# Optimization experiments

Measured on AMD Instinct MI355X. Metric: run time of the kernel, lower is better.

## Reference

```python
import jax, jax.numpy as jnp
import numpy as np
import math

VOCAB = 50257
DIM = 2048
R = 64
SCALING = 128.0 / math.sqrt(R)  # use_rslora=True -> alpha/sqrt(r) = 16.0


def setup_inputs() -> dict:
    key = jax.random.key(0)
    k1, k2, k3 = jax.random.split(key, 3)
    x = jax.random.randint(k1, (4, 4096), 0, VOCAB)
    weight = jax.random.normal(k2, (VOCAB, DIM), dtype=jnp.float32)
    # lora_A init: normal(0, 1/sqrt(r)); lora_B init: zeros (use randn here so
    # the LoRA path is numerically exercised)
    lora_A = jax.random.normal(k3, (R, VOCAB), dtype=jnp.float32) / math.sqrt(R)
    lora_B = jax.random.normal(jax.random.fold_in(key, 7), (DIM, R), dtype=jnp.float32) * 0.02
    return {"x": x, "weight": weight, "lora_A": lora_A, "lora_B": lora_B}


def reference(x, weight, lora_A, lora_B):
    # base embedding gather: [B, S, D]
    base_embed = weight[x]
    # Mathematically identical to F.embedding(x, (lora_B @ lora_A).T):
    # gather columns of lora_A by token id, then project with lora_B.
    a_rows = lora_A.T[x]                       # [B, S, r]
    lora_embed = jnp.einsum('bsr,dr->bsd', a_rows, lora_B)  # [B, S, D]
    return base_embed + lora_embed * SCALING
```

## Files before the change

kernel.cpp:

```cpp
#include <hip/hip_runtime.h>


constexpr int VOCAB = 50257;
constexpr int DIM = 2048;
constexpr int R = 64;
constexpr float SCALING = 16.0f;
constexpr int T_TILE = 64;
constexpr int BLOCK = 256;

__global__ void gather_a_kernel(const int* __restrict__ x,
                                const float* __restrict__ lora_A,
                                float* __restrict__ a_rows,
                                int n_tokens) {
  int gid = blockIdx.x * blockDim.x + threadIdx.x;
  if (gid >= n_tokens * R) return;
  int t = gid >> 6;
  int r = gid & (R - 1);
  int tok = x[t];
  a_rows[gid] = lora_A[(size_t)r * VOCAB + (size_t)tok];
}

template <bool USE_WS>
__global__ void fused_kernel(const int* __restrict__ x,
                             const float* __restrict__ weight,
                             const float* __restrict__ lora_A,
                             const float* __restrict__ a_rows,
                             const float* __restrict__ lora_B,
                             float* __restrict__ out) {
  const int d = blockIdx.y * BLOCK + threadIdx.x;
  const int t0 = blockIdx.x * T_TILE;

  float b[R];
  const float* bp = lora_B + (size_t)d * R;
#pragma unroll
  for (int i = 0; i < R; i += 4) {
    float4 v = *reinterpret_cast<const float4*>(bp + i);
    b[i] = v.x; b[i + 1] = v.y; b[i + 2] = v.z; b[i + 3] = v.w;
  }

#pragma unroll 1
  for (int tt = 0; tt < T_TILE; ++tt) {
    const int t = t0 + tt;
    const int tok = x[t];

    float a0 = 0.f, a1 = 0.f, a2 = 0.f, a3 = 0.f;
    if (USE_WS) {
      const float* ap = a_rows + (size_t)t * R;
#pragma unroll
      for (int r = 0; r < R; r += 4) {
        a0 += ap[r + 0] * b[r + 0];
        a1 += ap[r + 1] * b[r + 1];
        a2 += ap[r + 2] * b[r + 2];
        a3 += ap[r + 3] * b[r + 3];
      }
    } else {
#pragma unroll
      for (int r = 0; r < R; r += 4) {
        a0 += lora_A[(size_t)(r + 0) * VOCAB + tok] * b[r + 0];
        a1 += lora_A[(size_t)(r + 1) * VOCAB + tok] * b[r + 1];
        a2 += lora_A[(size_t)(r + 2) * VOCAB + tok] * b[r + 2];
        a3 += lora_A[(size_t)(r + 3) * VOCAB + tok] * b[r + 3];
      }
    }
    const float acc = (a0 + a1) + (a2 + a3);

    const float w = weight[(size_t)tok * DIM + d];
    out[(size_t)t * DIM + d] = w + SCALING * acc;
  }
}

extern "C" void kernel_launch(void* const* d_in, const int* in_sizes, int n_in,
                              void* d_out, int out_size, void* d_ws, size_t ws_size,
                              hipStream_t stream) {
  const int* x = (const int*)d_in[0];
  const float* weight = (const float*)d_in[1];
  const float* lora_A = (const float*)d_in[2];
  const float* lora_B = (const float*)d_in[3];
  float* out = (float*)d_out;

  const int n_tokens = in_sizes[0];
  const size_t ws_need = (size_t)n_tokens * R * sizeof(float);
  const bool use_ws = (d_ws != nullptr) && (ws_size >= ws_need);

  dim3 grid(n_tokens / T_TILE, DIM / BLOCK);

  if (use_ws) {
    float* a_rows = (float*)d_ws;
    const int total = n_tokens * R;
    gather_a_kernel<<<(total + BLOCK - 1) / BLOCK, BLOCK, 0, stream>>>(
        x, lora_A, a_rows, n_tokens);
    fused_kernel<true><<<grid, BLOCK, 0, stream>>>(
        x, weight, lora_A, a_rows, lora_B, out);
  } else {
    fused_kernel<false><<<grid, BLOCK, 0, stream>>>(
        x, weight, lora_A, nullptr, lora_B, out);
  }
}
```

Baseline: 689.8 us.

## Stage LoRA A tile in shared memory and split tokens across waves

Loads the gathered A rows and token ids for a 64-token tile into LDS, then each wave processes 16 tokens for a 64-wide slice of D using float4 LDS broadcasts and an unrolled loop. This is meant to replace per-thread global scalar loads of A and the serialized token→weight dependency with more memory-level parallelism. The D tile shrinks to 64, so A tiles are reloaded more often and B loads are per-block, and the workspace-less fallback is removed.

```diff
diff --git a/kernel.cpp b/kernel.cpp
--- a/kernel.cpp
+++ b/kernel.cpp
@@ -5,7 +5,10 @@
 constexpr int DIM = 2048;
 constexpr int R = 64;
 constexpr float SCALING = 16.0f;
+
 constexpr int T_TILE = 64;
+constexpr int D_TILE = 64;
+constexpr int WAVE_T = 16;
 constexpr int BLOCK = 256;
 
 __global__ void gather_a_kernel(const int* __restrict__ x,
@@ -20,52 +23,61 @@
   a_rows[gid] = lora_A[(size_t)r * VOCAB + (size_t)tok];
 }
 
-template <bool USE_WS>
-__global__ void fused_kernel(const int* __restrict__ x,
-                             const float* __restrict__ weight,
-                             const float* __restrict__ lora_A,
-                             const float* __restrict__ a_rows,
-                             const float* __restrict__ lora_B,
-                             float* __restrict__ out) {
-  const int d = blockIdx.y * BLOCK + threadIdx.x;
+__global__ __launch_bounds__(BLOCK) void fused_kernel(
+    const int* __restrict__ x,
+    const float* __restrict__ weight,
+    const float* __restrict__ a_rows,
+    const float* __restrict__ lora_B,
+    float* __restrict__ out) {
+  __shared__ float sA[T_TILE * R];
+  __shared__ int sTok[T_TILE];
+
+  const int tid = threadIdx.x;
+  const int wave = tid >> 6;
+  const int lane = tid & 63;
+  const int d = blockIdx.y * D_TILE + lane;
   const int t0 = blockIdx.x * T_TILE;
 
-  float b[R];
-  const float* bp = lora_B + (size_t)d * R;
+  if (tid < T_TILE) sTok[tid] = x[t0 + tid];
+  {
+    const float4* __restrict__ src =
+        reinterpret_cast<const float4*>(a_rows + (size_t)t0 * R);
+    float4* dst = reinterpret_cast<float4*>(sA);
 #pragma unroll
-  for (int i = 0; i < R; i += 4) {
-    float4 v = *reinterpret_cast<const float4*>(bp + i);
-    b[i] = v.x; b[i + 1] = v.y; b[i + 2] = v.z; b[i + 3] = v.w;
+    for (int i = 0; i < 4; ++i) dst[tid + BLOCK * i] = src[tid + BLOCK * i];
   }
 
-#pragma unroll 1
-  for (int tt = 0; tt < T_TILE; ++tt) {
-    const int t = t0 + tt;
-    const int tok = x[t];
+  float b[R];
+  {
+    const float4* __restrict__ bp =
+        reinterpret_cast<const float4*>(lora_B + (size_t)d * R);
+#pragma unroll
+    for (int i = 0; i < R / 4; ++i) {
+      float4 v = bp[i];
+      b[4 * i] = v.x; b[4 * i + 1] = v.y; b[4 * i + 2] = v.z; b[4 * i + 3] = v.w;
+    }
+  }
+  __syncthreads();
 
+  const int twbase = wave * WAVE_T;
+
+#pragma unroll 4
+  for (int tt = 0; tt < WAVE_T; ++tt) {
+    const int tloc = twbase + tt;
+    const int tok = sTok[tloc];
+    const float w = weight[(size_t)tok * DIM + d];
+    const float* __restrict__ a = sA + tloc * R;
     float a0 = 0.f, a1 = 0.f, a2 = 0.f, a3 = 0.f;
-    if (USE_WS) {
-      const float* ap = a_rows + (size_t)t * R;
 #pragma unroll
-      for (int r = 0; r < R; r += 4) {
-        a0 += ap[r + 0] * b[r + 0];
-        a1 += ap[r + 1] * b[r + 1];
-        a2 += ap[r + 2] * b[r + 2];
-        a3 += ap[r + 3] * b[r + 3];
-      }
-    } else {
-#pragma unroll
-      for (int r = 0; r < R; r += 4) {
-        a0 += lora_A[(size_t)(r + 0) * VOCAB + tok] * b[r + 0];
-        a1 += lora_A[(size_t)(r + 1) * VOCAB + tok] * b[r + 1];
-        a2 += lora_A[(size_t)(r + 2) * VOCAB + tok] * b[r + 2];
-        a3 += lora_A[(size_t)(r + 3) * VOCAB + tok] * b[r + 3];
-      }
+    for (int r = 0; r < R; r += 4) {
+      float4 av = *reinterpret_cast<const float4*>(a + r);
+      a0 += av.x * b[r + 0];
+      a1 += av.y * b[r + 1];
+      a2 += av.z * b[r + 2];
+      a3 += av.w * b[r + 3];
     }
     const float acc = (a0 + a1) + (a2 + a3);
-
-    const float w = weight[(size_t)tok * DIM + d];
-    out[(size_t)t * DIM + d] = w + SCALING * acc;
+    out[(size_t)(t0 + tloc) * DIM + d] = w + SCALING * acc;
   }
 }
 
@@ -79,20 +91,12 @@
   float* out = (float*)d_out;
 
   const int n_tokens = in_sizes[0];
-  const size_t ws_need = (size_t)n_tokens * R * sizeof(float);
-  const bool use_ws = (d_ws != nullptr) && (ws_size >= ws_need);
+  float* a_rows = (float*)d_ws;
 
-  dim3 grid(n_tokens / T_TILE, DIM / BLOCK);
+  const int total = n_tokens * R;
+  gather_a_kernel<<<(total + BLOCK - 1) / BLOCK, BLOCK, 0, stream>>>(
+      x, lora_A, a_rows, n_tokens);
 
-  if (use_ws) {
-    float* a_rows = (float*)d_ws;
-    const int total = n_tokens * R;
-    gather_a_kernel<<<(total + BLOCK - 1) / BLOCK, BLOCK, 0, stream>>>(
-        x, lora_A, a_rows, n_tokens);
-    fused_kernel<true><<<grid, BLOCK, 0, stream>>>(
-        x, weight, lora_A, a_rows, lora_B, out);
-  } else {
-    fused_kernel<false><<<grid, BLOCK, 0, stream>>>(
-        x, weight, lora_A, nullptr, lora_B, out);
-  }
+  dim3 grid(n_tokens / T_TILE, DIM / D_TILE);
+  fused_kernel<<<grid, BLOCK, 0, stream>>>(x, weight, a_rows, lora_B, out);
 }
```

After: 647.9 us. 6.1% less time.
